# Kernel tuning notes

Hardware: AMD Instinct MI355X
Metric: run time of the kernel (lower is better)

The kernel has to match this reference:

```python
import jax, jax.numpy as jnp
import numpy as np

N_USERS = 100_000
N_ITEMS = 100_000
D = 64            # args.in_size == args.out_size (GraphConv has weight=None)
N_INTENTS = 128   # hardcoded in DCCF
HID = 128         # SemanticAttention hidden_size
N_UI_EDGES = 1_000_000
N_MP_EDGES = 500_000
N_MP = 2          # metapaths per node type
B = 4096
N_LAYERS = 2      # hardcoded in DCCF


def setup_inputs() -> dict:
    key = jax.random.key(0)
    ks = jax.random.split(key, 20)
    s = 0.1
    inp = {}
    inp['user_feat'] = jax.random.normal(ks[0], (N_USERS, D), jnp.float32) * s
    inp['item_feat'] = jax.random.normal(ks[1], (N_ITEMS, D), jnp.float32) * s
    inp['user_intent'] = jax.random.normal(ks[2], (D, N_INTENTS), jnp.float32) * s
    inp['item_intent'] = jax.random.normal(ks[3], (D, N_INTENTS), jnp.float32) * s
    inp['sa_u_W1'] = jax.random.normal(ks[4], (D, HID), jnp.float32) * s
    inp['sa_u_b1'] = jnp.zeros((HID,), jnp.float32)
    inp['sa_u_w2'] = jax.random.normal(ks[5], (HID,), jnp.float32) * s
    inp['sa_i_W1'] = jax.random.normal(ks[6], (D, HID), jnp.float32) * s
    inp['sa_i_b1'] = jnp.zeros((HID,), jnp.float32)
    inp['sa_i_w2'] = jax.random.normal(ks[7], (HID,), jnp.float32) * s
    inp['ui_src'] = jax.random.randint(ks[8], (N_UI_EDGES,), 0, N_USERS)
    inp['ui_dst'] = jax.random.randint(ks[9], (N_UI_EDGES,), 0, N_ITEMS)
    inp['mp_user'] = jax.random.randint(ks[10], (N_MP, 2, N_MP_EDGES), 0, N_USERS)
    inp['mp_item'] = jax.random.randint(ks[11], (N_MP, 2, N_MP_EDGES), 0, N_ITEMS)
    # indices drawn WITHOUT replacement so torch.unique(index) in ssl_loss is a no-op
    inp['user_idx'] = jax.random.choice(ks[12], N_USERS, (B,), replace=False)
    inp['item_idx'] = jax.random.choice(ks[13], N_ITEMS, (B,), replace=False)
    inp['neg_item_idx'] = jax.random.randint(ks[14], (B,), 0, N_ITEMS)
    return inp


def _forward(user_feat, item_feat, user_intent, item_intent,
             sa_u_W1, sa_u_b1, sa_u_w2, sa_i_W1, sa_i_b1, sa_i_w2,
             ui_src, ui_dst, mp_user, mp_item, user_idx, item_idx, neg_item_idx):
    n_nodes = N_USERS + N_ITEMS
    # symmetric bipartite adjacency in COO (tmp_adj + tmp_adj.T)
    rows = jnp.concatenate([ui_src, ui_dst + N_USERS])
    cols = jnp.concatenate([ui_dst + N_USERS, ui_src])
    deg = jnp.maximum(jax.ops.segment_sum(jnp.ones_like(rows, jnp.float32), rows,
                                          num_segments=n_nodes), 1.0)
    dinv = jax.lax.rsqrt(deg)
    gv = dinv[rows] * dinv[cols]  # G = D^{-1/2} A D^{-1/2}

    def spmm(x):  # gather-scale-scatter, the torch_sparse.spmm
        return jax.ops.segment_sum(gv[:, None] * x[cols], rows, num_segments=n_nodes)

    # ---- DCCF ----
    emb = jnp.concatenate([user_feat, item_feat], axis=0)
    total = emb
    for _ in range(N_LAYERS):
        gnn = spmm(emb)
        u, it = emb[:N_USERS], emb[N_USERS:]
        u_int = jax.nn.softmax(u @ user_intent, axis=1) @ user_intent.T
        i_int = jax.nn.softmax(it @ item_intent, axis=1) @ item_intent.T
        emb = gnn + jnp.concatenate([u_int, i_int], axis=0) + emb
        total = total + emb  # torch.stack(...).sum(dim=1)
    ua, ia = total[:N_USERS], total[N_USERS:]

    # ---- HANLayer: GraphConv(norm='both', weight=None) per metapath ----
    def graphconv(src, dst, h, n):
        ones = jnp.ones_like(src, jnp.float32)
        outdeg = jnp.maximum(jax.ops.segment_sum(ones, src, num_segments=n), 1.0)
        indeg = jnp.maximum(jax.ops.segment_sum(ones, dst, num_segments=n), 1.0)
        x = h * jax.lax.rsqrt(outdeg)[:, None]
        agg = jax.ops.segment_sum(x[src], dst, num_segments=n)
        return agg * jax.lax.rsqrt(indeg)[:, None]

    def sem_att(z, W1, b1, w2):  # z: [N, M, D]
        w = jnp.mean(jnp.tanh(z @ W1 + b1) @ w2, axis=0)  # [M]
        beta = jax.nn.softmax(w)
        return jnp.einsum('m,nmd->nd', beta, z)

    zu = jnp.stack([graphconv(mp_user[m, 0], mp_user[m, 1], user_feat, N_USERS)
                    for m in range(N_MP)], axis=1)
    h2_u = sem_att(zu, sa_u_W1, sa_u_b1, sa_u_w2)
    zi = jnp.stack([graphconv(mp_item[m, 0], mp_item[m, 1], item_feat, N_ITEMS)
                    for m in range(N_MP)], axis=1)
    h2_i = sem_att(zi, sa_i_W1, sa_i_b1, sa_i_w2)

    user_emb = 0.5 * ua + 0.5 * h2_u
    item_emb = 0.5 * ia + 0.5 * h2_i

    def ssl(d1, d2, idx):  # InfoNCE with temp 0.5 (idx already unique)
        e1 = d1[idx]
        e2 = d2[idx]
        e1 = e1 / jnp.linalg.norm(e1, axis=1, keepdims=True)
        e2 = e2 / jnp.linalg.norm(e2, axis=1, keepdims=True)
        pos = jnp.sum(e1 * e2, axis=1) / 0.5
        lse = jax.nn.logsumexp(e1 @ e2.T / 0.5, axis=1)
        return -jnp.sum(pos - lse) / idx.shape[0]

    ssl_loss = ssl(h2_u, ua, user_idx) + ssl(h2_i, ia, item_idx)
    return (user_emb[user_idx], item_emb[item_idx], item_emb[neg_item_idx], ssl_loss)


def reference(user_feat, item_feat, user_intent, item_intent,
              sa_u_W1, sa_u_b1, sa_u_w2, sa_i_W1, sa_i_b1, sa_i_w2,
              ui_src, ui_dst, mp_user, mp_item, user_idx, item_idx, neg_item_idx):
    return _forward(user_feat, item_feat, user_intent, item_intent,
                    sa_u_W1, sa_u_b1, sa_u_w2, sa_i_W1, sa_i_b1, sa_i_w2,
                    ui_src, ui_dst, mp_user, mp_item, user_idx, item_idx, neg_item_idx)
```

## Files before the change

### kernel.cpp

```cpp
#include <hip/hip_runtime.h>
#include <math.h>

#define NUSERS   100000
#define NITEMS   100000
#define NNODES   200000
#define DD       64
#define NI       128
#define E_UI     1000000
#define E_MP     500000
#define BB       4096
#define NSTRIP   6250

#define O_CNT       0LL
#define O_OUTCNT    600000LL
#define O_CURSOR    1000000LL
#define O_PARTIALS  1600000LL
#define O_UITB_U    1625600LL
#define O_UITB_I    1629696LL
#define O_UIB_U     1633792LL
#define O_UIB_I     1637888LL
#define O_W1B_U     1641984LL
#define O_W1B_I     1646080LL
#define O_SUMEXP    1700000LL
#define O_POS       1708192LL
#define ZEND        1716384LL
#define O_OFF       1716384LL
#define O_BSUM      2316448LL
#define O_DINV      2317472LL
#define O_OINV      2517472LL
#define O_IINV      2917472LL
#define O_ADJ       3317472LL
#define O_WSUM      7317472LL
#define O_EMBA      7317480LL
#define O_TOTAL     20117480LL
#define O_EMBB      32917480LL
#define O_E1U       45717480LL
#define O_E2U       45979624LL
#define O_E1I       46241768LL
#define O_E2I       46503912LL

typedef __attribute__((ext_vector_type(8))) short short8;
typedef __attribute__((ext_vector_type(4))) float f32x4;

__device__ __forceinline__ short f2bf(float x) {
  unsigned u = __float_as_uint(x);
  unsigned r = (u + 0x7FFFu + ((u >> 16) & 1u)) >> 16;
  return (short)r;
}

__global__ void k_hist_main(const int* __restrict__ src, const int* __restrict__ dst,
                            int* __restrict__ cnt) {
  int e = blockIdx.x * 256 + threadIdx.x;
  if (e < E_UI) {
    atomicAdd(&cnt[src[e]], 1);
    atomicAdd(&cnt[NUSERS + dst[e]], 1);
  }
}

__global__ void k_hist_mp(const int* __restrict__ mpu, const int* __restrict__ mpi,
                          int* __restrict__ cnt, int* __restrict__ outcnt) {
  int e = blockIdx.x * 256 + threadIdx.x;
  int g = blockIdx.y;
  if (e < E_MP) {
    const int* base = (g < 2) ? (mpu + (long long)g * 2 * E_MP)
                              : (mpi + (long long)(g - 2) * 2 * E_MP);
    int s = base[e];
    int d = base[E_MP + e];
    atomicAdd(&outcnt[g * NUSERS + s], 1);
    atomicAdd(&cnt[NNODES + g * NUSERS + d], 1);
  }
}

__global__ __launch_bounds__(1024) void k_scan1(const int* __restrict__ in, int* __restrict__ out,
                                                int* __restrict__ bsum, int n) {
  __shared__ int s[1024];
  int i = blockIdx.x * 1024 + threadIdx.x;
  int v = (i < n) ? in[i] : 0;
  s[threadIdx.x] = v;
  __syncthreads();
  for (int off = 1; off < 1024; off <<= 1) {
    int x = (threadIdx.x >= off) ? s[threadIdx.x - off] : 0;
    __syncthreads();
    s[threadIdx.x] += x;
    __syncthreads();
  }
  if (i < n) out[i] = s[threadIdx.x] - v;
  if (threadIdx.x == 1023) bsum[blockIdx.x] = s[1023];
}

__global__ __launch_bounds__(1024) void k_scan2(int* __restrict__ bsum, int nb) {
  __shared__ int s[1024];
  int v = (threadIdx.x < nb) ? bsum[threadIdx.x] : 0;
  s[threadIdx.x] = v;
  __syncthreads();
  for (int off = 1; off < 1024; off <<= 1) {
    int x = (threadIdx.x >= off) ? s[threadIdx.x - off] : 0;
    __syncthreads();
    s[threadIdx.x] += x;
    __syncthreads();
  }
  if (threadIdx.x < nb) bsum[threadIdx.x] = s[threadIdx.x] - v;
}

__global__ __launch_bounds__(1024) void k_scan3(int* __restrict__ out, const int* __restrict__ bsum, int n) {
  int i = blockIdx.x * 1024 + threadIdx.x;
  if (i < n) out[i] += bsum[blockIdx.x];
}

__global__ void k_inv(const int* __restrict__ cnt, const int* __restrict__ outcnt,
                      float* __restrict__ dinv, float* __restrict__ iinv, float* __restrict__ oinv) {
  int i = blockIdx.x * 256 + threadIdx.x;
  if (i < NNODES) {
    int c = cnt[i]; if (c < 1) c = 1;
    dinv[i] = 1.0f / sqrtf((float)c);
  } else if (i < 600000) {
    int c = cnt[i]; if (c < 1) c = 1;
    iinv[i - NNODES] = 1.0f / sqrtf((float)c);
  }
  if (i < 400000) {
    int c = outcnt[i]; if (c < 1) c = 1;
    oinv[i] = 1.0f / sqrtf((float)c);
  }
}

__global__ void k_scatter_main(const int* __restrict__ src, const int* __restrict__ dst,
                               const int* __restrict__ off, int* __restrict__ cursor,
                               int* __restrict__ adj) {
  int e = blockIdx.x * 256 + threadIdx.x;
  if (e < E_UI) {
    int u = src[e];
    int it = NUSERS + dst[e];
    int p = atomicAdd(&cursor[u], 1);
    adj[off[u] + p] = it;
    int q = atomicAdd(&cursor[it], 1);
    adj[off[it] + q] = u;
  }
}

__global__ void k_scatter_mp(const int* __restrict__ mpu, const int* __restrict__ mpi,
                             const int* __restrict__ off, int* __restrict__ cursor,
                             int* __restrict__ adj) {
  int e = blockIdx.x * 256 + threadIdx.x;
  int g = blockIdx.y;
  if (e < E_MP) {
    const int* base = (g < 2) ? (mpu + (long long)g * 2 * E_MP)
                              : (mpi + (long long)(g - 2) * 2 * E_MP);
    int s = base[e];
    int d = base[E_MP + e];
    int node = NNODES + g * NUSERS + d;
    int p = atomicAdd(&cursor[node], 1);
    adj[off[node] + p] = s;
  }
}

__global__ void k_init(const float4* __restrict__ uf, const float4* __restrict__ itf,
                       float4* __restrict__ emb) {
  int i = blockIdx.x * 256 + threadIdx.x;
  if (i < 3200000) {
    emb[i] = (i < 1600000) ? uf[i] : itf[i - 1600000];
  }
}

__global__ void k_tw(const float* __restrict__ UIu, const float* __restrict__ UIi,
                     const float* __restrict__ W1u, const float* __restrict__ W1i,
                     short* __restrict__ UITBu, short* __restrict__ UITBi,
                     short* __restrict__ UIBu,  short* __restrict__ UIBi,
                     short* __restrict__ W1Bu,  short* __restrict__ W1Bi) {
  int t = blockIdx.x * 256 + threadIdx.x;
  if (t < 8192) {
    int d = t >> 7, j = t & 127;
    UITBu[j * 64 + d] = f2bf(UIu[t]);
    UITBi[j * 64 + d] = f2bf(UIi[t]);
    UIBu[t] = f2bf(UIu[t]);
    UIBi[t] = f2bf(UIi[t]);
    W1Bu[j * 64 + d] = f2bf(W1u[t]);
    W1Bi[j * 64 + d] = f2bf(W1i[t]);
  }
}

__device__ __forceinline__ float acc8(const float* __restrict__ tbl, int miv, float mwv,
                                      int rem, int lane, float acc) {
  unsigned wb = __float_as_uint(mwv);
  for (int k = 0; k < rem; k += 8) {
    int n0 = __builtin_amdgcn_readlane(miv, k + 0);
    int n1 = __builtin_amdgcn_readlane(miv, k + 1);
    int n2 = __builtin_amdgcn_readlane(miv, k + 2);
    int n3 = __builtin_amdgcn_readlane(miv, k + 3);
    int n4 = __builtin_amdgcn_readlane(miv, k + 4);
    int n5 = __builtin_amdgcn_readlane(miv, k + 5);
    int n6 = __builtin_amdgcn_readlane(miv, k + 6);
    int n7 = __builtin_amdgcn_readlane(miv, k + 7);
    float w0 = __uint_as_float(__builtin_amdgcn_readlane(wb, k + 0));
    float w1 = __uint_as_float(__builtin_amdgcn_readlane(wb, k + 1));
    float w2 = __uint_as_float(__builtin_amdgcn_readlane(wb, k + 2));
    float w3 = __uint_as_float(__builtin_amdgcn_readlane(wb, k + 3));
    float w4 = __uint_as_float(__builtin_amdgcn_readlane(wb, k + 4));
    float w5 = __uint_as_float(__builtin_amdgcn_readlane(wb, k + 5));
    float w6 = __uint_as_float(__builtin_amdgcn_readlane(wb, k + 6));
    float w7 = __uint_as_float(__builtin_amdgcn_readlane(wb, k + 7));
    float v0 = tbl[((long long)n0 << 6) + lane], v1 = tbl[((long long)n1 << 6) + lane];
    float v2 = tbl[((long long)n2 << 6) + lane], v3 = tbl[((long long)n3 << 6) + lane];
    float v4 = tbl[((long long)n4 << 6) + lane], v5 = tbl[((long long)n5 << 6) + lane];
    float v6 = tbl[((long long)n6 << 6) + lane], v7 = tbl[((long long)n7 << 6) + lane];
    acc += w0 * v0; acc += w1 * v1; acc += w2 * v2; acc += w3 * v3;
    acc += w4 * v4; acc += w5 * v5; acc += w6 * v6; acc += w7 * v7;
  }
  return acc;
}

template <int R>
__device__ __forceinline__ float acc8f(const float* __restrict__ tbl, int miv, float mwv,
                                       int lane) {
  unsigned wb = __float_as_uint(mwv);
  float acc = 0.0f;
#pragma unroll
  for (int k = 0; k < R; k += 8) {
    int n0 = __builtin_amdgcn_readlane(miv, k + 0);
    int n1 = __builtin_amdgcn_readlane(miv, k + 1);
    int n2 = __builtin_amdgcn_readlane(miv, k + 2);
    int n3 = __builtin_amdgcn_readlane(miv, k + 3);
    int n4 = __builtin_amdgcn_readlane(miv, k + 4);
    int n5 = __builtin_amdgcn_readlane(miv, k + 5);
    int n6 = __builtin_amdgcn_readlane(miv, k + 6);
    int n7 = __builtin_amdgcn_readlane(miv, k + 7);
    float w0 = __uint_as_float(__builtin_amdgcn_readlane(wb, k + 0));
    float w1 = __uint_as_float(__builtin_amdgcn_readlane(wb, k + 1));
    float w2 = __uint_as_float(__builtin_amdgcn_readlane(wb, k + 2));
    float w3 = __uint_as_float(__builtin_amdgcn_readlane(wb, k + 3));
    float w4 = __uint_as_float(__builtin_amdgcn_readlane(wb, k + 4));
    float w5 = __uint_as_float(__builtin_amdgcn_readlane(wb, k + 5));
    float w6 = __uint_as_float(__builtin_amdgcn_readlane(wb, k + 6));
    float w7 = __uint_as_float(__builtin_amdgcn_readlane(wb, k + 7));
    float v0 = tbl[((long long)n0 << 6) + lane], v1 = tbl[((long long)n1 << 6) + lane];
    float v2 = tbl[((long long)n2 << 6) + lane], v3 = tbl[((long long)n3 << 6) + lane];
    float v4 = tbl[((long long)n4 << 6) + lane], v5 = tbl[((long long)n5 << 6) + lane];
    float v6 = tbl[((long long)n6 << 6) + lane], v7 = tbl[((long long)n7 << 6) + lane];
    acc += w0 * v0; acc += w1 * v1; acc += w2 * v2; acc += w3 * v3;
    acc += w4 * v4; acc += w5 * v5; acc += w6 * v6; acc += w7 * v7;
  }
  return acc;
}

__device__ __forceinline__ float gather_tail(const float* __restrict__ tbl,
                                             const int* __restrict__ adj,
                                             int start, int c,
                                             const float* __restrict__ warr, int wofs,
                                             int lane, float acc) {
  for (int kb = 64; kb < c; kb += 64) {
    int rem = c - kb; if (rem > 64) rem = 64;
    int ti = 0; float tw = 0.0f;
    if (lane < rem) { ti = adj[start + kb + lane]; tw = warr[wofs + ti]; }
    acc = acc8(tbl, ti, tw, rem, lane, acc);
  }
  return acc;
}

__device__ __forceinline__ float gather_node(const float* __restrict__ tbl,
                                             const int* __restrict__ adj,
                                             int ofs, int c, int miv, float mwv,
                                             const float* __restrict__ warr, int wofs,
                                             int lane) {
  if (c <= 8)  return acc8f<8>(tbl, miv, mwv, lane);
  if (c <= 16) return acc8f<16>(tbl, miv, mwv, lane);
  if (c <= 24) return acc8f<24>(tbl, miv, mwv, lane);
  int rem = c < 64 ? c : 64;
  float acc = acc8(tbl, miv, mwv, rem, lane, 0.0f);
  if (c > 64) acc = gather_tail(tbl, adj, ofs, c, warr, wofs, lane, acc);
  return acc;
}

__device__ __forceinline__ float bcastf(float x) {
  return __uint_as_float(__builtin_amdgcn_readfirstlane(__float_as_uint(x)));
}

__global__ __launch_bounds__(128, 4) void k_layer(
    const float* __restrict__ ecur, float* __restrict__ enext, float* __restrict__ total,
    const int* __restrict__ adj, const int* __restrict__ off, const int* __restrict__ cnt,
    const float* __restrict__ dinv,
    const short* __restrict__ UITBu, const short* __restrict__ UITBi,
    const short* __restrict__ UIBu,  const short* __restrict__ UIBi, int layer) {
  __shared__ float sZ[2][16 * 68];
  __shared__ short sP[2][16 * 136];
  int w = threadIdx.x >> 6, lane = threadIdx.x & 63;
  int nb = blockIdx.x * 32 + w * 16;
  const short* UITB = (nb < NUSERS) ? UITBu : UITBi;
  const short* UIB  = (nb < NUSERS) ? UIBu  : UIBi;
  float* rowZ = sZ[w];
  short* rowP = sP[w];
  int quad = lane >> 4, mrow = lane & 15;

  const float* vrow = ecur + (((long long)(nb + mrow)) << 6) + quad * 8;
  float4 va0 = *(const float4*)(vrow);
  float4 va1 = *(const float4*)(vrow + 4);
  float4 vc0 = *(const float4*)(vrow + 32);
  float4 vc1 = *(const float4*)(vrow + 36);
  short8 a0 = { f2bf(va0.x), f2bf(va0.y), f2bf(va0.z), f2bf(va0.w),
                f2bf(va1.x), f2bf(va1.y), f2bf(va1.z), f2bf(va1.w) };
  short8 a1 = { f2bf(vc0.x), f2bf(vc0.y), f2bf(vc0.z), f2bf(vc0.w),
                f2bf(vc1.x), f2bf(vc1.y), f2bf(vc1.z), f2bf(vc1.w) };

  {
    int ofs[16], cns[16];
    float dn[16];
    int mi[16]; float mw[16];
    int cmax = 0;
#pragma unroll
    for (int m = 0; m < 16; m++) {
      ofs[m] = __builtin_amdgcn_readfirstlane(off[nb + m]);
      cns[m] = __builtin_amdgcn_readfirstlane(cnt[nb + m]);
      dn[m]  = bcastf(dinv[nb + m]);
      cmax = cns[m] > cmax ? cns[m] : cmax;
    }
#pragma unroll
    for (int m = 0; m < 16; m++)
      mi[m] = (lane < cns[m]) ? adj[ofs[m] + lane] : 0;
#pragma unroll
    for (int m = 0; m < 16; m++)
      mw[m] = (lane < cns[m]) ? dinv[mi[m]] : 0.0f;

    if (cmax <= 16) {
#pragma unroll
      for (int m = 0; m < 16; m++) {
        float acc = acc8f<16>(ecur, mi[m], mw[m], lane);
        rowZ[m * 68 + lane] = dn[m] * acc;
      }
    } else if (cmax <= 24) {
#pragma unroll
      for (int m = 0; m < 16; m++) {
        float acc = acc8f<24>(ecur, mi[m], mw[m], lane);
        rowZ[m * 68 + lane] = dn[m] * acc;
      }
    } else {
#pragma unroll
      for (int m = 0; m < 16; m++) {
        float acc = gather_node(ecur, adj, ofs[m], cns[m], mi[m], mw[m], dinv, 0, lane);
        rowZ[m * 68 + lane] = dn[m] * acc;
      }
    }
  }

  float den0 = 0.f, den1 = 0.f, den2 = 0.f, den3 = 0.f;
  short* pw = rowP + (quad * 4) * 136 + mrow;
#pragma unroll
  for (int jt = 0; jt < 8; jt++) {
    const short* wr = UITB + ((jt * 16 + mrow) << 6) + quad * 8;
    short8 b0 = *(const short8*)(wr);
    short8 bh = *(const short8*)(wr + 32);
    f32x4 acc = {0.f, 0.f, 0.f, 0.f};
    acc = __builtin_amdgcn_mfma_f32_16x16x32_bf16(a0, b0, acc, 0, 0, 0);
    acc = __builtin_amdgcn_mfma_f32_16x16x32_bf16(a1, bh, acc, 0, 0, 0);
    float e0 = __expf(acc[0]), e1 = __expf(acc[1]);
    float e2 = __expf(acc[2]), e3 = __expf(acc[3]);
    den0 += e0; den1 += e1; den2 += e2; den3 += e3;
    short* pj = pw + jt * 16;
    pj[0] = f2bf(e0); pj[136] = f2bf(e1); pj[272] = f2bf(e2); pj[408] = f2bf(e3);
  }
  for (int mask = 1; mask <= 8; mask <<= 1) {
    den0 += __shfl_xor(den0, mask); den1 += __shfl_xor(den1, mask);
    den2 += __shfl_xor(den2, mask); den3 += __shfl_xor(den3, mask);
  }
  float rd0 = 1.f / den0, rd1 = 1.f / den1, rd2 = 1.f / den2, rd3 = 1.f / den3;

#pragma unroll
  for (int dt = 0; dt < 4; dt++) {
    f32x4 acc = {0.f, 0.f, 0.f, 0.f};
#pragma unroll
    for (int c = 0; c < 4; c++) {
      const short* pr = rowP + mrow * 136 + c * 32 + quad * 8;
      short8 af = *(const short8*)(pr);
      const short* br = UIB + ((dt * 16 + mrow) << 7) + c * 32 + quad * 8;
      short8 bf = *(const short8*)(br);
      acc = __builtin_amdgcn_mfma_f32_16x16x32_bf16(af, bf, acc, 0, 0, 0);
    }
    int d = dt * 16 + mrow;
#define COMB(r, rd)                                                            \
    { int node = nb + quad * 4 + r;                                            \
      long long base = (((long long)node) << 6) + d;                           \
      float o = acc[r] * rd;                                                   \
      float gn = rowZ[(quad * 4 + r) * 68 + d];                                \
      float vv = ecur[base];                                                   \
      float ne = gn + o + vv;                                                  \
      enext[base] = ne;                                                        \
      total[base] = (layer == 0) ? (vv + ne) : (total[base] + ne); }
    COMB(0, rd0) COMB(1, rd1) COMB(2, rd2) COMB(3, rd3)
#undef COMB
  }
}

__global__ __launch_bounds__(128, 4) void k_mp_fused(
    const float* __restrict__ uf, const float* __restrict__ itf,
    const int* __restrict__ adj, const int* __restrict__ off, const int* __restrict__ cnt,
    const float* __restrict__ oinv, const float* __restrict__ iinv,
    float* __restrict__ zu, float* __restrict__ zi,
    const short* __restrict__ W1Bu, const float* __restrict__ b1u, const float* __restrict__ w2u,
    const short* __restrict__ W1Bi, const float* __restrict__ b1i, const float* __restrict__ w2i,
    float* __restrict__ partials) {
  __shared__ float sZ[2][16 * 68];
  int g = blockIdx.y;
  const float* feat = (g < 2) ? uf : itf;
  float* zb = (g < 2) ? zu + ((long long)g * NUSERS << 6)
                      : zi + ((long long)(g - 2) * NUSERS << 6);
  const short* W1B = (g < 2) ? W1Bu : W1Bi;
  const float* b1  = (g < 2) ? b1u : b1i;
  const float* w2  = (g < 2) ? w2u : w2i;
  int w = threadIdx.x >> 6, lane = threadIdx.x & 63;
  int strip = blockIdx.x * 2 + w;
  int nb = strip * 16;
  int gofs = g * NUSERS;
  float* rowZ = sZ[w];

  {
    int ofs[16], cns[16];
    float dn[16];
    int mi[16]; float mw[16];
    int cmax = 0;
#pragma unroll
    for (int m = 0; m < 16; m++) {
      int node = NNODES + gofs + nb + m;
      ofs[m] = __builtin_amdgcn_readfirstlane(off[node]);
      cns[m] = __builtin_amdgcn_readfirstlane(cnt[node]);
      dn[m]  = bcastf(iinv[gofs + nb + m]);
      cmax = cns[m] > cmax ? cns[m] : cmax;
    }
#pragma unroll
    for (int m = 0; m < 16; m++)
      mi[m] = (lane < cns[m]) ? adj[ofs[m] + lane] : 0;
#pragma unroll
    for (int m = 0; m < 16; m++)
      mw[m] = (lane < cns[m]) ? oinv[gofs + mi[m]] : 0.0f;

    if (cmax <= 8) {
#pragma unroll
      for (int m = 0; m < 16; m++) {
        float zv = dn[m] * acc8f<8>(feat, mi[m], mw[m], lane);
        rowZ[m * 68 + lane] = zv;
        zb[((long long)(nb + m) << 6) + lane] = zv;
      }
    } else if (cmax <= 16) {
#pragma unroll
      for (int m = 0; m < 16; m++) {
        float zv = dn[m] * acc8f<16>(feat, mi[m], mw[m], lane);
        rowZ[m * 68 + lane] = zv;
        zb[((long long)(nb + m) << 6) + lane] = zv;
      }
    } else {
#pragma unroll
      for (int m = 0; m < 16; m++) {
        float zv = dn[m] * gather_node(feat, adj, ofs[m], cns[m], mi[m], mw[m],
                                       oinv, gofs, lane);
        rowZ[m * 68 + lane] = zv;
        zb[((long long)(nb + m) << 6) + lane] = zv;
      }
    }
  }

  int quad = lane >> 4, mrow = lane & 15;
  const float* zrow = rowZ + mrow * 68 + quad * 8;
  short8 a0 = { f2bf(zrow[0]), f2bf(zrow[1]), f2bf(zrow[2]), f2bf(zrow[3]),
                f2bf(zrow[4]), f2bf(zrow[5]), f2bf(zrow[6]), f2bf(zrow[7]) };
  short8 a1 = { f2bf(zrow[32]), f2bf(zrow[33]), f2bf(zrow[34]), f2bf(zrow[35]),
                f2bf(zrow[36]), f2bf(zrow[37]), f2bf(zrow[38]), f2bf(zrow[39]) };
  float psum = 0.0f;
#pragma unroll
  for (int jt = 0; jt < 8; jt++) {
    const short* wr = W1B + ((jt * 16 + mrow) << 6) + quad * 8;
    short8 b0 = *(const short8*)(wr);
    short8 bh = *(const short8*)(wr + 32);
    f32x4 acc = {0.f, 0.f, 0.f, 0.f};
    acc = __builtin_amdgcn_mfma_f32_16x16x32_bf16(a0, b0, acc, 0, 0, 0);
    acc = __builtin_amdgcn_mfma_f32_16x16x32_bf16(a1, bh, acc, 0, 0, 0);
    int j = jt * 16 + mrow;
    float bj = b1[j], wj = w2[j];
#pragma unroll
    for (int r = 0; r < 4; r++) {
      float s = acc[r] + bj;
      psum += wj * (1.0f - 2.0f / (__expf(2.0f * s) + 1.0f));
    }
  }
  for (int m = 32; m; m >>= 1) psum += __shfl_xor(psum, m);
  if (lane == 0) partials[g * NSTRIP + strip] = psum;
}

__global__ void k_beta(const float* __restrict__ partials, float* __restrict__ wsum) {
  int g = blockIdx.x;
  float s = 0.0f;
  for (int i = threadIdx.x; i < NSTRIP; i += 256) s += partials[g * NSTRIP + i];
  for (int m = 32; m; m >>= 1) s += __shfl_xor(s, m);
  __shared__ float r[4];
  if ((threadIdx.x & 63) == 0) r[threadIdx.x >> 6] = s;
  __syncthreads();
  if (threadIdx.x == 0) wsum[g] = r[0] + r[1] + r[2] + r[3];
}

__global__ __launch_bounds__(256) void k_h2out(
    const float* __restrict__ zu, const float* __restrict__ zi,
    const int* __restrict__ user_idx, const int* __restrict__ item_idx, const int* __restrict__ neg_idx,
    const float* __restrict__ total,
    const float* __restrict__ wsum, float* __restrict__ out,
    short* __restrict__ e1u, short* __restrict__ e2u,
    short* __restrict__ e1i, short* __restrict__ e2i, float* __restrict__ pos) {
  int lane = threadIdx.x & 63;
  int row = (blockIdx.x << 2) + (threadIdx.x >> 6);
  int seg = row >> 12;
  int r = row & 4095;
  int idx;
  const float* zb;
  int gbase;
  if (seg == 0)      { idx = user_idx[r]; zb = zu; gbase = 0; }
  else if (seg == 1) { idx = item_idx[r]; zb = zi; gbase = 2; }
  else               { idx = neg_idx[r];  zb = zi; gbase = 2; }
  int tnode = gbase ? (NUSERS + idx) : idx;
  float t = total[((long long)tnode << 6) + lane];
  float w0 = wsum[gbase] * (1.0f / 100000.0f);
  float w1 = wsum[gbase + 1] * (1.0f / 100000.0f);
  float mb = fmaxf(w0, w1);
  float b0 = expf(w0 - mb), b1 = expf(w1 - mb);
  float bs = b0 + b1;
  b0 /= bs; b1 /= bs;
  float z0 = zb[((long long)idx << 6) + lane];
  float z1 = zb[(((long long)NUSERS + idx) << 6) + lane];
  float h2 = b0 * z0 + b1 * z1;
  out[((long long)row << 6) + lane] = 0.5f * t + 0.5f * h2;
  if (seg < 2) {
    float n1 = h2 * h2, n2 = t * t;
    for (int m = 32; m; m >>= 1) { n1 += __shfl_xor(n1, m); n2 += __shfl_xor(n2, m); }
    n1 = sqrtf(n1); n2 = sqrtf(n2);
    float a = h2 / n1, b = t / n2;
    float d = a * b;
    for (int m = 32; m; m >>= 1) d += __shfl_xor(d, m);
    short* e1 = seg ? e1i : e1u;
    short* e2 = seg ? e2i : e2u;
    e1[((long long)r << 6) + lane] = f2bf(a);
    e2[((long long)r << 6) + lane] = f2bf(b);
    if (lane == 0) pos[seg * BB + r] = 2.0f * d;
  }
}

__global__ __launch_bounds__(256) void k_gemm(const short* __restrict__ e1u, const short* __restrict__ e2u,
                                              const short* __restrict__ e1i, const short* __restrict__ e2i,
                                              float* __restrict__ sumexp) {
  int side = blockIdx.z;
  const short* A = side ? e1i : e1u;
  const short* B = side ? e2i : e2u;
  int w = threadIdx.x >> 6, lane = threadIdx.x & 63;
  int quad = lane >> 4, mrow = lane & 15;
  int rbase = blockIdx.y * 64;
  int cbase = blockIdx.x * 256 + w * 64;

  short8 a0[4], a1[4], b0[4], b1[4];
#pragma unroll
  for (int ri = 0; ri < 4; ri++) {
    const short* ar = A + ((long long)(rbase + ri * 16 + mrow) << 6) + quad * 8;
    a0[ri] = *(const short8*)ar;
    a1[ri] = *(const short8*)(ar + 32);
  }
#pragma unroll
  for (int ci = 0; ci < 4; ci++) {
    const short* br = B + ((long long)(cbase + ci * 16 + mrow) << 6) + quad * 8;
    b0[ci] = *(const short8*)br;
    b1[ci] = *(const short8*)(br + 32);
  }
  float rs0[4] = {0.f, 0.f, 0.f, 0.f};
  float rs1[4] = {0.f, 0.f, 0.f, 0.f};
  float rs2[4] = {0.f, 0.f, 0.f, 0.f};
  float rs3[4] = {0.f, 0.f, 0.f, 0.f};
#pragma unroll
  for (int ri = 0; ri < 4; ri++) {
#pragma unroll
    for (int ci = 0; ci < 4; ci++) {
      f32x4 acc = {0.f, 0.f, 0.f, 0.f};
      acc = __builtin_amdgcn_mfma_f32_16x16x32_bf16(a0[ri], b0[ci], acc, 0, 0, 0);
      acc = __builtin_amdgcn_mfma_f32_16x16x32_bf16(a1[ri], b1[ci], acc, 0, 0, 0);
      float e0 = __expf(2.0f * acc[0]);
      float e1 = __expf(2.0f * acc[1]);
      float e2 = __expf(2.0f * acc[2]);
      float e3 = __expf(2.0f * acc[3]);
      if (ri == 0) { rs0[0] += e0; rs0[1] += e1; rs0[2] += e2; rs0[3] += e3; }
      if (ri == 1) { rs1[0] += e0; rs1[1] += e1; rs1[2] += e2; rs1[3] += e3; }
      if (ri == 2) { rs2[0] += e0; rs2[1] += e1; rs2[2] += e2; rs2[3] += e3; }
      if (ri == 3) { rs3[0] += e0; rs3[1] += e1; rs3[2] += e2; rs3[3] += e3; }
    }
  }
#pragma unroll
  for (int mask = 1; mask <= 8; mask <<= 1) {
#pragma unroll
    for (int r = 0; r < 4; r++) {
      rs0[r] += __shfl_xor(rs0[r], mask);
      rs1[r] += __shfl_xor(rs1[r], mask);
      rs2[r] += __shfl_xor(rs2[r], mask);
      rs3[r] += __shfl_xor(rs3[r], mask);
    }
  }
  if (mrow == 0) {
    float* sb = sumexp + side * BB + rbase + quad * 4;
#pragma unroll
    for (int r = 0; r < 4; r++) {
      __hip_atomic_fetch_add(&sb[r], rs0[r], __ATOMIC_RELAXED, __HIP_MEMORY_SCOPE_AGENT);
      __hip_atomic_fetch_add(&sb[16 + r], rs1[r], __ATOMIC_RELAXED, __HIP_MEMORY_SCOPE_AGENT);
      __hip_atomic_fetch_add(&sb[32 + r], rs2[r], __ATOMIC_RELAXED, __HIP_MEMORY_SCOPE_AGENT);
      __hip_atomic_fetch_add(&sb[48 + r], rs3[r], __ATOMIC_RELAXED, __HIP_MEMORY_SCOPE_AGENT);
    }
  }
}

__global__ void k_loss(const float* __restrict__ sumexp, const float* __restrict__ pos,
                       float* __restrict__ out) {
  float s = 0.0f;
  for (int i = threadIdx.x; i < 2 * BB; i += 256) s += logf(sumexp[i]) - pos[i];
  for (int m = 32; m; m >>= 1) s += __shfl_xor(s, m);
  __shared__ float r[4];
  if ((threadIdx.x & 63) == 0) r[threadIdx.x >> 6] = s;
  __syncthreads();
  if (threadIdx.x == 0) out[3 * BB * DD] = (r[0] + r[1] + r[2] + r[3]) * (1.0f / (float)BB);
}

extern "C" void kernel_launch(void* const* d_in, const int* in_sizes, int n_in,
                              void* d_out, int out_size, void* d_ws, size_t ws_size,
                              hipStream_t stream) {
  const float* uf  = (const float*)d_in[0];
  const float* itf = (const float*)d_in[1];
  const float* UIu = (const float*)d_in[2];
  const float* UIi = (const float*)d_in[3];
  const float* W1u = (const float*)d_in[4];
  const float* b1u = (const float*)d_in[5];
  const float* w2u = (const float*)d_in[6];
  const float* W1i = (const float*)d_in[7];
  const float* b1i = (const float*)d_in[8];
  const float* w2i = (const float*)d_in[9];
  const int* ui_src   = (const int*)d_in[10];
  const int* ui_dst   = (const int*)d_in[11];
  const int* mpu      = (const int*)d_in[12];
  const int* mpi      = (const int*)d_in[13];
  const int* user_idx = (const int*)d_in[14];
  const int* item_idx = (const int*)d_in[15];
  const int* neg_idx  = (const int*)d_in[16];
  float* out = (float*)d_out;

  float* wf = (float*)d_ws;
  int*   wi = (int*)d_ws;

  int*   cnt      = wi + O_CNT;
  int*   outcnt   = wi + O_OUTCNT;
  int*   cursor   = wi + O_CURSOR;
  float* partials = wf + O_PARTIALS;
  short* UITBu    = (short*)(wf + O_UITB_U);
  short* UITBi    = (short*)(wf + O_UITB_I);
  short* UIBu     = (short*)(wf + O_UIB_U);
  short* UIBi     = (short*)(wf + O_UIB_I);
  short* W1Bu     = (short*)(wf + O_W1B_U);
  short* W1Bi     = (short*)(wf + O_W1B_I);
  float* sumexp   = wf + O_SUMEXP;
  float* pos      = wf + O_POS;
  int*   off      = wi + O_OFF;
  int*   bsum     = wi + O_BSUM;
  float* dinv     = wf + O_DINV;
  float* oinv     = wf + O_OINV;
  float* iinv     = wf + O_IINV;
  int*   adj      = wi + O_ADJ;
  float* wsum     = wf + O_WSUM;
  float* emba     = wf + O_EMBA;
  float* total    = wf + O_TOTAL;
  float* embb     = wf + O_EMBB;
  short* e1u      = (short*)(wf + O_E1U);
  short* e2u      = (short*)(wf + O_E2U);
  short* e1i      = (short*)(wf + O_E1I);
  short* e2i      = (short*)(wf + O_E2I);

  hipMemsetAsync(d_ws, 0, (size_t)ZEND * 4, stream);

  k_hist_main<<<(E_UI + 255) / 256, 256, 0, stream>>>(ui_src, ui_dst, cnt);
  k_hist_mp<<<dim3((E_MP + 255) / 256, 4), 256, 0, stream>>>(mpu, mpi, cnt, outcnt);

  const int NSCAN = 600000;
  const int NB = (NSCAN + 1023) / 1024;
  k_scan1<<<NB, 1024, 0, stream>>>(cnt, off, bsum, NSCAN);
  k_scan2<<<1, 1024, 0, stream>>>(bsum, NB);
  k_scan3<<<NB, 1024, 0, stream>>>(off, bsum, NSCAN);

  k_inv<<<(600000 + 255) / 256, 256, 0, stream>>>(cnt, outcnt, dinv, iinv, oinv);

  k_scatter_main<<<(E_UI + 255) / 256, 256, 0, stream>>>(ui_src, ui_dst, off, cursor, adj);
  k_scatter_mp<<<dim3((E_MP + 255) / 256, 4), 256, 0, stream>>>(mpu, mpi, off, cursor, adj);

  k_init<<<(3200000 + 255) / 256, 256, 0, stream>>>((const float4*)uf, (const float4*)itf,
                                                    (float4*)emba);
  k_tw<<<32, 256, 0, stream>>>(UIu, UIi, W1u, W1i, UITBu, UITBi, UIBu, UIBi, W1Bu, W1Bi);

  k_layer<<<6250, 128, 0, stream>>>(emba, embb, total, adj, off, cnt, dinv,
                                    UITBu, UITBi, UIBu, UIBi, 0);
  k_layer<<<6250, 128, 0, stream>>>(embb, emba, total, adj, off, cnt, dinv,
                                    UITBu, UITBi, UIBu, UIBi, 1);

  k_mp_fused<<<dim3(3125, 4), 128, 0, stream>>>(uf, itf, adj, off, cnt, oinv, iinv,
                                                emba, embb,
                                                W1Bu, b1u, w2u, W1Bi, b1i, w2i, partials);
  k_beta<<<4, 256, 0, stream>>>(partials, wsum);

  k_h2out<<<3072, 256, 0, stream>>>(emba, embb, user_idx, item_idx, neg_idx, total,
                                    wsum, out, e1u, e2u, e1i, e2i, pos);

  k_gemm<<<dim3(16, 64, 2), 256, 0, stream>>>(e1u, e2u, e1i, e2i, sumexp);
  k_loss<<<1, 256, 0, stream>>>(sumexp, pos, out);
}
```

Baseline: 1.101 ms.

## Recompute metapath aggregates for batch rows instead of storing full z buffers

The fused metapath kernel no longer writes the full per-node metapath aggregates (4 x 100k x 64 floats) to global memory. The output kernel instead regathers the two metapath neighbourhoods for only the 12k batch rows it needs. The two histogram kernels are merged into one launch, and so are the two scatter kernels, using a grid y-dimension. This removes a large write stream and two launches, at the cost of redundant gathers in k_h2out and a grid where 4 of 5 y-slices of blocks are partially idle.

```diff
diff --git a/kernel.cpp b/kernel.cpp
--- a/kernel.cpp
+++ b/kernel.cpp
@@ -48,26 +48,26 @@
   return (short)r;
 }
 
-__global__ void k_hist_main(const int* __restrict__ src, const int* __restrict__ dst,
-                            int* __restrict__ cnt) {
-  int e = blockIdx.x * 256 + threadIdx.x;
-  if (e < E_UI) {
-    atomicAdd(&cnt[src[e]], 1);
-    atomicAdd(&cnt[NUSERS + dst[e]], 1);
-  }
-}
-
-__global__ void k_hist_mp(const int* __restrict__ mpu, const int* __restrict__ mpi,
-                          int* __restrict__ cnt, int* __restrict__ outcnt) {
+__global__ void k_hist(const int* __restrict__ src, const int* __restrict__ dst,
+                       const int* __restrict__ mpu, const int* __restrict__ mpi,
+                       int* __restrict__ cnt, int* __restrict__ outcnt) {
   int e = blockIdx.x * 256 + threadIdx.x;
   int g = blockIdx.y;
-  if (e < E_MP) {
-    const int* base = (g < 2) ? (mpu + (long long)g * 2 * E_MP)
-                              : (mpi + (long long)(g - 2) * 2 * E_MP);
-    int s = base[e];
-    int d = base[E_MP + e];
-    atomicAdd(&outcnt[g * NUSERS + s], 1);
-    atomicAdd(&cnt[NNODES + g * NUSERS + d], 1);
+  if (g == 0) {
+    if (e < E_UI) {
+      atomicAdd(&cnt[src[e]], 1);
+      atomicAdd(&cnt[NUSERS + dst[e]], 1);
+    }
+  } else {
+    int gg = g - 1;
+    if (e < E_MP) {
+      const int* base = (gg < 2) ? (mpu + (long long)gg * 2 * E_MP)
+                                 : (mpi + (long long)(gg - 2) * 2 * E_MP);
+      int s = base[e];
+      int d = base[E_MP + e];
+      atomicAdd(&outcnt[gg * NUSERS + s], 1);
+      atomicAdd(&cnt[NNODES + gg * NUSERS + d], 1);
+    }
   }
 }
 
@@ -123,33 +123,32 @@
   }
 }
 
-__global__ void k_scatter_main(const int* __restrict__ src, const int* __restrict__ dst,
-                               const int* __restrict__ off, int* __restrict__ cursor,
-                               int* __restrict__ adj) {
-  int e = blockIdx.x * 256 + threadIdx.x;
-  if (e < E_UI) {
-    int u = src[e];
-    int it = NUSERS + dst[e];
-    int p = atomicAdd(&cursor[u], 1);
-    adj[off[u] + p] = it;
-    int q = atomicAdd(&cursor[it], 1);
-    adj[off[it] + q] = u;
-  }
-}
-
-__global__ void k_scatter_mp(const int* __restrict__ mpu, const int* __restrict__ mpi,
-                             const int* __restrict__ off, int* __restrict__ cursor,
-                             int* __restrict__ adj) {
+__global__ void k_scatter(const int* __restrict__ src, const int* __restrict__ dst,
+                          const int* __restrict__ mpu, const int* __restrict__ mpi,
+                          const int* __restrict__ off, int* __restrict__ cursor,
+                          int* __restrict__ adj) {
   int e = blockIdx.x * 256 + threadIdx.x;
   int g = blockIdx.y;
-  if (e < E_MP) {
-    const int* base = (g < 2) ? (mpu + (long long)g * 2 * E_MP)
-                              : (mpi + (long long)(g - 2) * 2 * E_MP);
-    int s = base[e];
-    int d = base[E_MP + e];
-    int node = NNODES + g * NUSERS + d;
-    int p = atomicAdd(&cursor[node], 1);
-    adj[off[node] + p] = s;
+  if (g == 0) {
+    if (e < E_UI) {
+      int u = src[e];
+      int it = NUSERS + dst[e];
+      int p = atomicAdd(&cursor[u], 1);
+      adj[off[u] + p] = it;
+      int q = atomicAdd(&cursor[it], 1);
+      adj[off[it] + q] = u;
+    }
+  } else {
+    int gg = g - 1;
+    if (e < E_MP) {
+      const int* base = (gg < 2) ? (mpu + (long long)gg * 2 * E_MP)
+                                 : (mpi + (long long)(gg - 2) * 2 * E_MP);
+      int s = base[e];
+      int d = base[E_MP + e];
+      int node = NNODES + gg * NUSERS + d;
+      int p = atomicAdd(&cursor[node], 1);
+      adj[off[node] + p] = s;
+    }
   }
 }
 
@@ -391,15 +390,12 @@
     const float* __restrict__ uf, const float* __restrict__ itf,
     const int* __restrict__ adj, const int* __restrict__ off, const int* __restrict__ cnt,
     const float* __restrict__ oinv, const float* __restrict__ iinv,
-    float* __restrict__ zu, float* __restrict__ zi,
     const short* __restrict__ W1Bu, const float* __restrict__ b1u, const float* __restrict__ w2u,
     const short* __restrict__ W1Bi, const float* __restrict__ b1i, const float* __restrict__ w2i,
     float* __restrict__ partials) {
   __shared__ float sZ[2][16 * 68];
   int g = blockIdx.y;
   const float* feat = (g < 2) ? uf : itf;
-  float* zb = (g < 2) ? zu + ((long long)g * NUSERS << 6)
-                      : zi + ((long long)(g - 2) * NUSERS << 6);
   const short* W1B = (g < 2) ? W1Bu : W1Bi;
   const float* b1  = (g < 2) ? b1u : b1i;
   const float* w2  = (g < 2) ? w2u : w2i;
@@ -431,26 +427,17 @@
 
     if (cmax <= 8) {
 #pragma unroll
-      for (int m = 0; m < 16; m++) {
-        float zv = dn[m] * acc8f<8>(feat, mi[m], mw[m], lane);
-        rowZ[m * 68 + lane] = zv;
-        zb[((long long)(nb + m) << 6) + lane] = zv;
-      }
+      for (int m = 0; m < 16; m++)
+        rowZ[m * 68 + lane] = dn[m] * acc8f<8>(feat, mi[m], mw[m], lane);
     } else if (cmax <= 16) {
 #pragma unroll
-      for (int m = 0; m < 16; m++) {
-        float zv = dn[m] * acc8f<16>(feat, mi[m], mw[m], lane);
-        rowZ[m * 68 + lane] = zv;
-        zb[((long long)(nb + m) << 6) + lane] = zv;
-      }
+      for (int m = 0; m < 16; m++)
+        rowZ[m * 68 + lane] = dn[m] * acc8f<16>(feat, mi[m], mw[m], lane);
     } else {
 #pragma unroll
-      for (int m = 0; m < 16; m++) {
-        float zv = dn[m] * gather_node(feat, adj, ofs[m], cns[m], mi[m], mw[m],
-                                       oinv, gofs, lane);
-        rowZ[m * 68 + lane] = zv;
-        zb[((long long)(nb + m) << 6) + lane] = zv;
-      }
+      for (int m = 0; m < 16; m++)
+        rowZ[m * 68 + lane] = dn[m] * gather_node(feat, adj, ofs[m], cns[m], mi[m], mw[m],
+                                                  oinv, gofs, lane);
     }
   }
 
@@ -493,7 +480,9 @@
 }
 
 __global__ __launch_bounds__(256) void k_h2out(
-    const float* __restrict__ zu, const float* __restrict__ zi,
+    const float* __restrict__ uf, const float* __restrict__ itf,
+    const int* __restrict__ adj, const int* __restrict__ off, const int* __restrict__ cnt,
+    const float* __restrict__ oinv, const float* __restrict__ iinv,
     const int* __restrict__ user_idx, const int* __restrict__ item_idx, const int* __restrict__ neg_idx,
     const float* __restrict__ total,
     const float* __restrict__ wsum, float* __restrict__ out,
@@ -504,21 +493,36 @@
   int seg = row >> 12;
   int r = row & 4095;
   int idx;
-  const float* zb;
   int gbase;
-  if (seg == 0)      { idx = user_idx[r]; zb = zu; gbase = 0; }
-  else if (seg == 1) { idx = item_idx[r]; zb = zi; gbase = 2; }
-  else               { idx = neg_idx[r];  zb = zi; gbase = 2; }
+  if (seg == 0)      { idx = user_idx[r]; gbase = 0; }
+  else if (seg == 1) { idx = item_idx[r]; gbase = 2; }
+  else               { idx = neg_idx[r];  gbase = 2; }
+  const float* feat = gbase ? itf : uf;
   int tnode = gbase ? (NUSERS + idx) : idx;
   float t = total[((long long)tnode << 6) + lane];
+
+  int g0ofs = gbase * NUSERS, g1ofs = (gbase + 1) * NUSERS;
+  int node0 = NNODES + g0ofs + idx;
+  int node1 = NNODES + g1ofs + idx;
+  int of0 = __builtin_amdgcn_readfirstlane(off[node0]);
+  int c0  = __builtin_amdgcn_readfirstlane(cnt[node0]);
+  int of1 = __builtin_amdgcn_readfirstlane(off[node1]);
+  int c1  = __builtin_amdgcn_readfirstlane(cnt[node1]);
+  float iv0 = bcastf(iinv[g0ofs + idx]);
+  float iv1 = bcastf(iinv[g1ofs + idx]);
+  int mi0 = (lane < c0) ? adj[of0 + lane] : 0;
+  int mi1 = (lane < c1) ? adj[of1 + lane] : 0;
+  float mw0 = (lane < c0) ? oinv[g0ofs + mi0] : 0.0f;
+  float mw1 = (lane < c1) ? oinv[g1ofs + mi1] : 0.0f;
+  float z0 = iv0 * gather_node(feat, adj, of0, c0, mi0, mw0, oinv, g0ofs, lane);
+  float z1 = iv1 * gather_node(feat, adj, of1, c1, mi1, mw1, oinv, g1ofs, lane);
+
   float w0 = wsum[gbase] * (1.0f / 100000.0f);
   float w1 = wsum[gbase + 1] * (1.0f / 100000.0f);
   float mb = fmaxf(w0, w1);
   float b0 = expf(w0 - mb), b1 = expf(w1 - mb);
   float bs = b0 + b1;
   b0 /= bs; b1 /= bs;
-  float z0 = zb[((long long)idx << 6) + lane];
-  float z1 = zb[(((long long)NUSERS + idx) << 6) + lane];
   float h2 = b0 * z0 + b1 * z1;
   out[((long long)row << 6) + lane] = 0.5f * t + 0.5f * h2;
   if (seg < 2) {
@@ -668,8 +672,8 @@
 
   hipMemsetAsync(d_ws, 0, (size_t)ZEND * 4, stream);
 
-  k_hist_main<<<(E_UI + 255) / 256, 256, 0, stream>>>(ui_src, ui_dst, cnt);
-  k_hist_mp<<<dim3((E_MP + 255) / 256, 4), 256, 0, stream>>>(mpu, mpi, cnt, outcnt);
+  k_hist<<<dim3((E_UI + 255) / 256, 5), 256, 0, stream>>>(ui_src, ui_dst, mpu, mpi,
+                                                          cnt, outcnt);
 
   const int NSCAN = 600000;
   const int NB = (NSCAN + 1023) / 1024;
@@ -679,8 +683,8 @@
 
   k_inv<<<(600000 + 255) / 256, 256, 0, stream>>>(cnt, outcnt, dinv, iinv, oinv);
 
-  k_scatter_main<<<(E_UI + 255) / 256, 256, 0, stream>>>(ui_src, ui_dst, off, cursor, adj);
-  k_scatter_mp<<<dim3((E_MP + 255) / 256, 4), 256, 0, stream>>>(mpu, mpi, off, cursor, adj);
+  k_scatter<<<dim3((E_UI + 255) / 256, 5), 256, 0, stream>>>(ui_src, ui_dst, mpu, mpi,
+                                                             off, cursor, adj);
 
   k_init<<<(3200000 + 255) / 256, 256, 0, stream>>>((const float4*)uf, (const float4*)itf,
                                                     (float4*)emba);
@@ -692,11 +696,11 @@
                                     UITBu, UITBi, UIBu, UIBi, 1);
 
   k_mp_fused<<<dim3(3125, 4), 128, 0, stream>>>(uf, itf, adj, off, cnt, oinv, iinv,
-                                                emba, embb,
                                                 W1Bu, b1u, w2u, W1Bi, b1i, w2i, partials);
   k_beta<<<4, 256, 0, stream>>>(partials, wsum);
 
-  k_h2out<<<3072, 256, 0, stream>>>(emba, embb, user_idx, item_idx, neg_idx, total,
+  k_h2out<<<3072, 256, 0, stream>>>(uf, itf, adj, off, cnt, oinv, iinv,
+                                    user_idx, item_idx, neg_idx, total,
                                     wsum, out, e1u, e2u, e1i, e2i, pos);
 
   k_gemm<<<dim3(16, 64, 2), 256, 0, stream>>>(e1u, e2u, e1i, e2i, sumexp);
```

Measured after the change: 1.140 ms. 3.5% more time.
